# Performance work log

Measured on AMD Instinct MI355X. Metric: run time of the kernel, lower is better.

Reference implementation:

```python
import jax, jax.numpy as jnp
import numpy as np

F8_MAX = 448.0   # max representable magnitude of float8_e4m3fn
EPS = 1e-12      # amax clamp from the source


def setup_inputs() -> dict:
    key = jax.random.key(0)
    kx, kw, kb = jax.random.split(key, 3)
    B, S, K, N = 8, 8192, 1024, 1024
    x = jax.random.normal(kx, (B, S, K), dtype=jnp.float32)
    weight = jax.random.normal(kw, (N, K), dtype=jnp.float32) * 0.02  # (out, in) like nn.Linear
    bias = jax.random.normal(kb, (N,), dtype=jnp.float32)
    return {"x": x, "weight": weight, "bias": bias}


def _quantize_fp8(t):
    """Per-tensor dynamic fp8-e4m3 quantization: returns (t_fp8, scale)."""
    scale = jnp.maximum(jnp.max(jnp.abs(t)), EPS) / F8_MAX
    t8 = (t / scale).astype(jnp.float8_e4m3fn)
    return t8, scale


def reference(x, weight, bias):
    lead = x.shape[:-1]
    K = x.shape[-1]
    N = weight.shape[0]
    x_flat = x.reshape(-1, K).astype(jnp.float32)

    # dynamic activation quantization (forward-time, per tensor)
    x8, x_scale = _quantize_fp8(x_flat)
    # weight quantization (from_linear, per tensor)
    w8, w_scale = _quantize_fp8(weight.astype(jnp.float32))

    out = jnp.dot(x8.astype(jnp.float32), w8.astype(jnp.float32).T) * (x_scale * w_scale)
    out = out.astype(x.dtype).reshape(*lead, N)
    return out + bias
```

## Files before the change

kernel.cpp:

```cpp
#include <hip/hip_runtime.h>
#include <stdint.h>

#define F8MAX 448.0f
#define QEPS 1e-12f
#define SCL_ONE 0x7F7F7F7F
#define AXB 4096

typedef float floatx16 __attribute__((ext_vector_type(16)));
typedef int   intx4    __attribute__((ext_vector_type(4)));
typedef int   intx8    __attribute__((ext_vector_type(8)));

__global__ __launch_bounds__(256) void amax_partial_xw(
    const float* __restrict__ x, int nx4,
    const float* __restrict__ w, int nw4,
    float* __restrict__ px, float* __restrict__ pw)
{
    const float4* x4 = (const float4*)x;
    const float4* w4 = (const float4*)w;
    int tid = blockIdx.x * 256 + threadIdx.x;
    int stride = gridDim.x * 256;
    float mx = 0.f, mw = 0.f;
    for (int i = tid; i < nx4; i += stride) {
        float4 v = x4[i];
        mx = fmaxf(mx, fmaxf(fmaxf(fabsf(v.x), fabsf(v.y)), fmaxf(fabsf(v.z), fabsf(v.w))));
    }
    for (int i = tid; i < nw4; i += stride) {
        float4 v = w4[i];
        mw = fmaxf(mw, fmaxf(fmaxf(fabsf(v.x), fabsf(v.y)), fmaxf(fabsf(v.z), fabsf(v.w))));
    }
    #pragma unroll
    for (int off = 32; off > 0; off >>= 1) {
        mx = fmaxf(mx, __shfl_xor(mx, off, 64));
        mw = fmaxf(mw, __shfl_xor(mw, off, 64));
    }
    __shared__ float smx[4], smw[4];
    if ((threadIdx.x & 63) == 0) { smx[threadIdx.x >> 6] = mx; smw[threadIdx.x >> 6] = mw; }
    __syncthreads();
    if (threadIdx.x == 0) {
        px[blockIdx.x] = fmaxf(fmaxf(smx[0], smx[1]), fmaxf(smx[2], smx[3]));
        pw[blockIdx.x] = fmaxf(fmaxf(smw[0], smw[1]), fmaxf(smw[2], smw[3]));
    }
}

__global__ __launch_bounds__(256) void quant_fused(
    const float* __restrict__ x, const float* __restrict__ w,
    uint8_t* __restrict__ x8, uint8_t* __restrict__ w8,
    const float* __restrict__ px, const float* __restrict__ pw,
    unsigned* __restrict__ hdr, int nhx, int nkt, int K)
{
    __shared__ uint8_t lds[65536];

    int bid = blockIdx.x;
    bool isw = (bid < 16);
    const float* par = isw ? pw : px;

    float m = 0.f;
    for (int i = threadIdx.x; i < AXB; i += 256) m = fmaxf(m, par[i]);
    #pragma unroll
    for (int off = 32; off > 0; off >>= 1) m = fmaxf(m, __shfl_xor(m, off, 64));
    __shared__ float red[4];
    if ((threadIdx.x & 63) == 0) red[threadIdx.x >> 6] = m;
    __syncthreads();
    float amax = fmaxf(fmaxf(red[0], red[1]), fmaxf(red[2], red[3]));

    float scale = fmaxf(amax, QEPS) / F8MAX;
    float rs = 1.0f / scale;

    if (threadIdx.x == 0) {
        if (bid == 0)  hdr[1] = __float_as_uint(amax);
        if (bid == 16) hdr[0] = __float_as_uint(amax);
    }

    int hp = isw ? bid : (nhx - 1 - (bid - 16));
    const float* src = isw ? w : x;
    uint8_t* dst8 = isw ? w8 : x8;
    int p = hp >> 1, half = hp & 1;

    int wave = threadIdx.x >> 6, lane = threadIdx.x & 63;
    int K4 = K >> 2;

    const float4* s4 = (const float4*)src + (size_t)(p * 128 + half * 64) * K4;
    uint32_t key = (lane >> 2) & 7;
    uint32_t lbase = ((uint32_t)(lane >> 4) * 4096) + (((lane >> 2) & 3) * 1024) + ((lane & 3) * 4);
    for (int rr = 0; rr < 16; rr++) {
        int r = rr * 4 + wave;
        const float4* rowp = s4 + (size_t)r * K4;
        #pragma unroll
        for (int j = 0; j < 4; j++) {
            float4 f = rowp[j * 64 + lane];
            int wd = 0;
            wd = __builtin_amdgcn_cvt_pk_fp8_f32(f.x * rs, f.y * rs, wd, false);
            wd = __builtin_amdgcn_cvt_pk_fp8_f32(f.z * rs, f.w * rs, wd, true);
            uint32_t a = (uint32_t)j * 16384 + lbase + (uint32_t)r * 16;
            a ^= (key << 4);
            *(int*)(lds + a) = wd;
        }
    }
    __syncthreads();

    uint8_t* outb = dst8 + (size_t)(p * nkt) * 8192 + half * 1024;
    for (int i = 0; i < 16; i++) {
        int c = i * 4 + wave;
        int kt = c >> 2, hpc = c & 3;
        uint32_t k2 = (uint32_t)(((kt & 1) << 2) | hpc);
        uint32_t a = (uint32_t)c * 1024 + (((uint32_t)lane * 16) ^ (k2 << 4));
        int4 v = *(const int4*)(lds + a);
        *(int4*)(outb + (size_t)kt * 8192 + hpc * 2048 + lane * 16) = v;
    }
}

__global__ __launch_bounds__(512, 1) void gemm_fp8_mx(
    const uint8_t* __restrict__ A8, const uint8_t* __restrict__ B8,
    float* __restrict__ C, const float* __restrict__ bias,
    const unsigned* __restrict__ hdr, int N, int nkt, int nbn)
{
    __shared__ uint8_t lsA[3 * 16384];
    __shared__ uint8_t lsB[3 * 16384];

    int nwg = gridDim.x;
    int bid = blockIdx.x;
    if ((nwg & 7) == 0) {
        int chunk = nwg >> 3;
        bid = (blockIdx.x & 7) * chunk + (blockIdx.x >> 3);
    }
    int bm = bid / nbn, bn = bid - bm * nbn;

    int t = threadIdx.x;
    int wave = t >> 6, lane = t & 63;
    int wr = wave >> 2, wc = wave & 3;
    int hl = lane >> 5, l31 = lane & 31;

    const uint8_t* gsrc0; const uint8_t* gsrc1; const uint8_t* gsrc2; const uint8_t* gsrc3;
    uint32_t ld0, ld1, ld2, ld3;
    bool isA = (wave < 4);
    {
        int c0 = wave * 4;
        #pragma unroll
        for (int p = 0; p < 4; p++) {
            int c = c0 + p;
            const uint8_t* g;
            uint32_t l;
            if (c < 16) {
                int h = c >> 3, sub = c & 7;
                g = A8 + (size_t)(bm * 2 + h) * nkt * 8192 + sub * 1024 + lane * 16;
                l = (uint32_t)c * 1024;
            } else {
                int cc = c - 16, h = cc >> 3, sub = cc & 7;
                g = B8 + (size_t)(bn * 2 + h) * nkt * 8192 + sub * 1024 + lane * 16;
                l = (uint32_t)cc * 1024;
            }
            if (p == 0) { gsrc0 = g; ld0 = l; }
            else if (p == 1) { gsrc1 = g; ld1 = l; }
            else if (p == 2) { gsrc2 = g; ld2 = l; }
            else { gsrc3 = g; ld3 = l; }
        }
    }
    uint8_t* lsbase = isA ? lsA : lsB;

#define ISSUE(GP, LO, KT2, B2)                                                   \
    __builtin_amdgcn_global_load_lds(                                            \
        (const __attribute__((address_space(1))) void*)((GP) + (size_t)(KT2) * 8192), \
        (__attribute__((address_space(3))) void*)(lsbase + (B2) * 16384 + (LO)), \
        16, 0, 0)

    const uint8_t* baseA = lsA + wr * 8192 + hl * 4096 + l31 * 16;
    const uint8_t* baseB = lsB + (wc >> 1) * 8192 + hl * 4096 + (wc & 1) * 1024 + l31 * 16;

    floatx16 acc[4][2];
    #pragma unroll
    for (int m = 0; m < 4; m++)
        #pragma unroll
        for (int n = 0; n < 2; n++)
            acc[m][n] = (floatx16)(0.0f);

#define RD8(BASE, OFF) __builtin_shufflevector(                         \
        *(const intx4*)((BASE) + (OFF)),                                \
        *(const intx4*)((BASE) + (OFF) + 2048), 0, 1, 2, 3, 4, 5, 6, 7)

#define MMX(m, n) acc[m][n] = __builtin_amdgcn_mfma_scale_f32_32x32x64_f8f6f4( \
        af[m], bf[n], acc[m][n], 0, 0, 0, SCL_ONE, 0, SCL_ONE)

    ISSUE(gsrc0, ld0, 0, 0); ISSUE(gsrc1, ld1, 0, 0); ISSUE(gsrc2, ld2, 0, 0); ISSUE(gsrc3, ld3, 0, 0);
    ISSUE(gsrc0, ld0, 1, 1); ISSUE(gsrc1, ld1, 1, 1); ISSUE(gsrc2, ld2, 1, 1); ISSUE(gsrc3, ld3, 1, 1);
    asm volatile("s_waitcnt vmcnt(4)" ::: "memory");
    asm volatile("s_barrier" ::: "memory");

    int cur = 0;
    for (int kt = 0; kt < nkt; kt++) {
        bool pf = (kt + 2 < nkt);
        int ib = cur - 1; if (ib < 0) ib += 3;
        const uint8_t* cA = baseA + cur * 16384;
        const uint8_t* cB = baseB + cur * 16384;
        intx8 af[4], bf[2];

        if (pf) { ISSUE(gsrc0, ld0, kt + 2, ib); ISSUE(gsrc1, ld1, kt + 2, ib);
                  ISSUE(gsrc2, ld2, kt + 2, ib); ISSUE(gsrc3, ld3, kt + 2, ib); }

        af[0] = RD8(cA, 0);    af[1] = RD8(cA, 512);
        bf[0] = RD8(cB, 0);    bf[1] = RD8(cB, 512);
        af[2] = RD8(cA, 1024); af[3] = RD8(cA, 1536);

        __builtin_amdgcn_s_setprio(1);
        MMX(0, 0); MMX(0, 1); MMX(1, 0); MMX(1, 1);
        MMX(2, 0); MMX(2, 1); MMX(3, 0); MMX(3, 1);
        __builtin_amdgcn_s_setprio(0);

        if (kt + 1 < nkt) {
            if (pf) asm volatile("s_waitcnt vmcnt(4)" ::: "memory");
            else    asm volatile("s_waitcnt vmcnt(0)" ::: "memory");
            asm volatile("s_barrier" ::: "memory");
        }
        cur++; if (cur == 3) cur = 0;
    }

    float sxv = fmaxf(__uint_as_float(hdr[0]), QEPS) / F8MAX;
    float swv = fmaxf(__uint_as_float(hdr[1]), QEPS) / F8MAX;
    float s = sxv * swv;

    #pragma unroll
    for (int m = 0; m < 4; m++) {
        int row0 = bm * 256 + wr * 128 + m * 32 + 4 * hl;
        #pragma unroll
        for (int n = 0; n < 2; n++) {
            int col = bn * 256 + wc * 64 + n * 32 + l31;
            float bv = bias[col];
            #pragma unroll
            for (int reg = 0; reg < 16; reg++) {
                int row = row0 + (reg & 3) + 8 * (reg >> 2);
                __builtin_nontemporal_store(acc[m][n][reg] * s + bv, &C[(size_t)row * N + col]);
            }
        }
    }
#undef ISSUE
#undef RD8
#undef MMX
}

extern "C" void kernel_launch(void* const* d_in, const int* in_sizes, int n_in,
                              void* d_out, int out_size, void* d_ws, size_t ws_size,
                              hipStream_t stream)
{
    const float* x    = (const float*)d_in[0];
    const float* w    = (const float*)d_in[1];
    const float* bias = (const float*)d_in[2];
    float* out = (float*)d_out;

    int N = in_sizes[2];
    int K = in_sizes[1] / N;
    int M = in_sizes[0] / K;
    int nx = in_sizes[0];
    int nw = in_sizes[1];
    int nkt = K / 64;

    uint8_t* ws = (uint8_t*)d_ws;
    unsigned* hdr = (unsigned*)ws;
    float* px = (float*)(ws + 64);
    float* pw = (float*)(ws + 64 + 16384);
    uint8_t* w8 = ws + 65536;
    uint8_t* x8 = ws + 65536 + (size_t)N * K;

    int nhx = (M / 128) * 2;
    int nhw = (N / 128) * 2;

    amax_partial_xw<<<AXB, 256, 0, stream>>>(x, nx / 4, w, nw / 4, px, pw);
    quant_fused<<<nhw + nhx, 256, 0, stream>>>(x, w, x8, w8, px, pw, hdr, nhx, nkt, K);

    int nbm = M / 256, nbn = N / 256;
    gemm_fp8_mx<<<nbm * nbn, 512, 0, stream>>>(x8, w8, out, bias, hdr, N, nkt, nbn);
}
```

Before: 219.2 us.

## Shrink GEMM tile to 256x128 with 4 waves, double buffering, two blocks per CU

The FP8 GEMM moves from a 256x256 output tile with 8 waves and a 3-stage LDS ring to a 256x128 tile with 4 waves and 2-stage double buffering. Launch bounds now allow two blocks per CU. The grid doubles, which is meant to give better occupancy and let one block's loads overlap another's compute. In exchange, B-tile reuse is lower, so more global traffic is needed per output. The shallower pipeline also waits on vmcnt(0) every iteration, which can expose load latency.

```diff
diff --git a/kernel.cpp b/kernel.cpp
--- a/kernel.cpp
+++ b/kernel.cpp
@@ -109,13 +109,12 @@
     }
 }
 
-__global__ __launch_bounds__(512, 1) void gemm_fp8_mx(
+__global__ __launch_bounds__(256, 2) void gemm_fp8_mx(
     const uint8_t* __restrict__ A8, const uint8_t* __restrict__ B8,
     float* __restrict__ C, const float* __restrict__ bias,
     const unsigned* __restrict__ hdr, int N, int nkt, int nbn)
 {
-    __shared__ uint8_t lsA[3 * 16384];
-    __shared__ uint8_t lsB[3 * 16384];
+    __shared__ uint8_t ls[2 * 24576];
 
     int nwg = gridDim.x;
     int bid = blockIdx.x;
@@ -127,44 +126,32 @@
 
     int t = threadIdx.x;
     int wave = t >> 6, lane = t & 63;
-    int wr = wave >> 2, wc = wave & 3;
+    int wr = wave >> 1, wc = wave & 1;
     int hl = lane >> 5, l31 = lane & 31;
 
-    const uint8_t* gsrc0; const uint8_t* gsrc1; const uint8_t* gsrc2; const uint8_t* gsrc3;
-    uint32_t ld0, ld1, ld2, ld3;
-    bool isA = (wave < 4);
-    {
-        int c0 = wave * 4;
-        #pragma unroll
-        for (int p = 0; p < 4; p++) {
-            int c = c0 + p;
-            const uint8_t* g;
-            uint32_t l;
-            if (c < 16) {
-                int h = c >> 3, sub = c & 7;
-                g = A8 + (size_t)(bm * 2 + h) * nkt * 8192 + sub * 1024 + lane * 16;
-                l = (uint32_t)c * 1024;
-            } else {
-                int cc = c - 16, h = cc >> 3, sub = cc & 7;
-                g = B8 + (size_t)(bn * 2 + h) * nkt * 8192 + sub * 1024 + lane * 16;
-                l = (uint32_t)cc * 1024;
-            }
-            if (p == 0) { gsrc0 = g; ld0 = l; }
-            else if (p == 1) { gsrc1 = g; ld1 = l; }
-            else if (p == 2) { gsrc2 = g; ld2 = l; }
-            else { gsrc3 = g; ld3 = l; }
-        }
-    }
-    uint8_t* lsbase = isA ? lsA : lsB;
-
-#define ISSUE(GP, LO, KT2, B2)                                                   \
+    const uint8_t* gs[6];
+    uint32_t lo[6];
+    #pragma unroll
+    for (int p = 0; p < 6; p++) {
+        int c = wave * 6 + p;
+        if (c < 16) {
+            int h = c >> 3, sub = c & 7;
+            gs[p] = A8 + (size_t)(bm * 2 + h) * nkt * 8192 + sub * 1024 + lane * 16;
+        } else {
+            int sub = c - 16;
+            gs[p] = B8 + (size_t)bn * nkt * 8192 + sub * 1024 + lane * 16;
+        }
+        lo[p] = (uint32_t)c * 1024;
+    }
+
+#define ISSUE(P, KT2, B2)                                                        \
     __builtin_amdgcn_global_load_lds(                                            \
-        (const __attribute__((address_space(1))) void*)((GP) + (size_t)(KT2) * 8192), \
-        (__attribute__((address_space(3))) void*)(lsbase + (B2) * 16384 + (LO)), \
+        (const __attribute__((address_space(1))) void*)(gs[P] + (size_t)(KT2) * 8192), \
+        (__attribute__((address_space(3))) void*)(ls + (B2) * 24576 + lo[P]),    \
         16, 0, 0)
 
-    const uint8_t* baseA = lsA + wr * 8192 + hl * 4096 + l31 * 16;
-    const uint8_t* baseB = lsB + (wc >> 1) * 8192 + hl * 4096 + (wc & 1) * 1024 + l31 * 16;
+    const uint8_t* baseA = ls + wr * 8192 + hl * 4096 + l31 * 16;
+    const uint8_t* baseB = ls + 16384 + hl * 4096 + wc * 1024 + l31 * 16;
 
     floatx16 acc[4][2];
     #pragma unroll
@@ -180,21 +167,21 @@
 #define MMX(m, n) acc[m][n] = __builtin_amdgcn_mfma_scale_f32_32x32x64_f8f6f4( \
         af[m], bf[n], acc[m][n], 0, 0, 0, SCL_ONE, 0, SCL_ONE)
 
-    ISSUE(gsrc0, ld0, 0, 0); ISSUE(gsrc1, ld1, 0, 0); ISSUE(gsrc2, ld2, 0, 0); ISSUE(gsrc3, ld3, 0, 0);
-    ISSUE(gsrc0, ld0, 1, 1); ISSUE(gsrc1, ld1, 1, 1); ISSUE(gsrc2, ld2, 1, 1); ISSUE(gsrc3, ld3, 1, 1);
-    asm volatile("s_waitcnt vmcnt(4)" ::: "memory");
+    #pragma unroll
+    for (int p = 0; p < 6; p++) ISSUE(p, 0, 0);
+    asm volatile("s_waitcnt vmcnt(0)" ::: "memory");
     asm volatile("s_barrier" ::: "memory");
 
-    int cur = 0;
+    int buf = 0;
     for (int kt = 0; kt < nkt; kt++) {
-        bool pf = (kt + 2 < nkt);
-        int ib = cur - 1; if (ib < 0) ib += 3;
-        const uint8_t* cA = baseA + cur * 16384;
-        const uint8_t* cB = baseB + cur * 16384;
+        bool pf = (kt + 1 < nkt);
+        if (pf) {
+            #pragma unroll
+            for (int p = 0; p < 6; p++) ISSUE(p, kt + 1, buf ^ 1);
+        }
+        const uint8_t* cA = baseA + buf * 24576;
+        const uint8_t* cB = baseB + buf * 24576;
         intx8 af[4], bf[2];
-
-        if (pf) { ISSUE(gsrc0, ld0, kt + 2, ib); ISSUE(gsrc1, ld1, kt + 2, ib);
-                  ISSUE(gsrc2, ld2, kt + 2, ib); ISSUE(gsrc3, ld3, kt + 2, ib); }
 
         af[0] = RD8(cA, 0);    af[1] = RD8(cA, 512);
         bf[0] = RD8(cB, 0);    bf[1] = RD8(cB, 512);
@@ -205,12 +192,11 @@
         MMX(2, 0); MMX(2, 1); MMX(3, 0); MMX(3, 1);
         __builtin_amdgcn_s_setprio(0);
 
-        if (kt + 1 < nkt) {
-            if (pf) asm volatile("s_waitcnt vmcnt(4)" ::: "memory");
-            else    asm volatile("s_waitcnt vmcnt(0)" ::: "memory");
+        if (pf) {
+            asm volatile("s_waitcnt vmcnt(0)" ::: "memory");
             asm volatile("s_barrier" ::: "memory");
         }
-        cur++; if (cur == 3) cur = 0;
+        buf ^= 1;
     }
 
     float sxv = fmaxf(__uint_as_float(hdr[0]), QEPS) / F8MAX;
@@ -222,7 +208,7 @@
         int row0 = bm * 256 + wr * 128 + m * 32 + 4 * hl;
         #pragma unroll
         for (int n = 0; n < 2; n++) {
-            int col = bn * 256 + wc * 64 + n * 32 + l31;
+            int col = bn * 128 + wc * 64 + n * 32 + l31;
             float bv = bias[col];
             #pragma unroll
             for (int reg = 0; reg < 16; reg++) {
@@ -265,6 +251,6 @@
     amax_partial_xw<<<AXB, 256, 0, stream>>>(x, nx / 4, w, nw / 4, px, pw);
     quant_fused<<<nhw + nhx, 256, 0, stream>>>(x, w, x8, w8, px, pw, hdr, nhx, nkt, K);
 
-    int nbm = M / 256, nbn = N / 256;
-    gemm_fp8_mx<<<nbm * nbn, 512, 0, stream>>>(x8, w8, out, bias, hdr, N, nkt, nbn);
-}
+    int nbm = M / 256, nbn = N / 128;
+    gemm_fp8_mx<<<nbm * nbn, 256, 0, stream>>>(x8, w8, out, bias, hdr, N, nkt, nbn);
+}
```

Result: slower. 241.0 us (+10.0%).
